# Kernel tuning notes

Hardware: AMD Instinct MI355X
Metric: run time of the kernel (lower is better)

## Reference

```python
import jax, jax.numpy as jnp
import numpy as np

D_MODEL = 1024
NUM_HEADS = 16
HEAD_DIM = D_MODEL // NUM_HEADS
B, S = 2, 2048


def setup_inputs() -> dict:
    key = jax.random.key(0)
    ks = jax.random.split(key, 6)
    scale = 0.02
    return {
        "x": jax.random.normal(ks[0], (B, S, D_MODEL), dtype=jnp.float32),
        "mask": jax.random.normal(ks[1], (S, S), dtype=jnp.float32),
        "Wqkv": jax.random.normal(ks[2], (D_MODEL, 3 * D_MODEL), dtype=jnp.float32) * scale,
        "bqkv": jax.random.normal(ks[3], (3 * D_MODEL,), dtype=jnp.float32) * scale,
        "Wout": jax.random.normal(ks[4], (D_MODEL, D_MODEL), dtype=jnp.float32) * scale,
        "bout": jax.random.normal(ks[5], (D_MODEL,), dtype=jnp.float32) * scale,
    }


def reference(x, mask, Wqkv, bqkv, Wout, bout):
    b, s, d = x.shape
    h, hd = NUM_HEADS, HEAD_DIM
    qkv = x @ Wqkv + bqkv                              # [b, s, 3d]
    qkv = qkv.reshape(b, s, h, 3 * hd).transpose(0, 2, 1, 3)  # [b, h, s, 3hd]
    q, k, v = jnp.split(qkv, 3, axis=-1)               # each [b, h, s, hd]
    scaled = jnp.einsum("bhqd,bhkd->bhqk", q, k) / jnp.sqrt(jnp.float32(hd))
    scaled = scaled + mask                             # mask [s, s] broadcasts
    attn = jax.nn.softmax(scaled, axis=-1)
    values = jnp.einsum("bhqk,bhkd->bhqd", attn, v)    # [b, h, s, hd]
    values = values.transpose(0, 2, 1, 3).reshape(b, s, d)
    return values @ Wout + bout
```

## Files before the change

kernel.cpp:

```cpp
#include <hip/hip_runtime.h>
#include <hip/hip_bf16.h>

#define D_MODEL 1024
#define NH 16
#define HD 64
#define BATCH 2
#define SEQ 2048
#define M_TOTAL (BATCH*SEQ)

typedef _Float16 f16;
typedef _Float16 half8 __attribute__((ext_vector_type(8)));
typedef _Float16 half4v __attribute__((ext_vector_type(4)));
typedef float floatx4 __attribute__((ext_vector_type(4)));

__device__ inline void gload_lds16(const void* g, void* l) {
    __builtin_amdgcn_global_load_lds(
        (const __attribute__((address_space(1))) unsigned int*)g,
        (__attribute__((address_space(3))) unsigned int*)l, 16, 0, 0);
}

__global__ void cvt_f32_f16(const float* __restrict__ src, f16* __restrict__ dst, int n4) {
    int i = blockIdx.x * blockDim.x + threadIdx.x;
    if (i < n4) {
        float4 v = ((const float4*)src)[i];
        half4v o = { (f16)v.x, (f16)v.y, (f16)v.z, (f16)v.w };
        *(half4v*)(dst + (long)i * 4) = o;
    }
}

__global__ void exp_cvt(const float* __restrict__ src, f16* __restrict__ dst, int n4) {
    int i = blockIdx.x * blockDim.x + threadIdx.x;
    if (i < n4) {
        float4 v = ((const float4*)src)[i];
        half4v o = { (f16)__expf(v.x), (f16)__expf(v.y), (f16)__expf(v.z), (f16)__expf(v.w) };
        *(half4v*)(dst + (long)i * 4) = o;
    }
}

__global__ void transpose_cvt(const float* __restrict__ src, f16* __restrict__ dst, int R, int C) {
    __shared__ float tile[32][33];
    int tx = threadIdx.x;
    int ty = threadIdx.y;
    int c0 = blockIdx.x * 32;
    int r0 = blockIdx.y * 32;
    for (int yy = 0; yy < 32; yy += 8)
        tile[ty + yy][tx] = src[(long)(r0 + ty + yy) * C + c0 + tx];
    __syncthreads();
    for (int yy = 0; yy < 32; yy += 8)
        dst[(long)(c0 + ty + yy) * R + r0 + tx] = (f16)tile[tx][ty + yy];
}

template<int MODE, int TN>
__global__ __launch_bounds__(256) void gemm_mfma(
    const f16* __restrict__ A, const f16* __restrict__ BT,
    const float* __restrict__ bias,
    f16* __restrict__ Qh, f16* __restrict__ Kh, f16* __restrict__ Vtg,
    float* __restrict__ out, int Kdim)
{
    constexpr int NF = TN / 32;
    __shared__ f16 Ah[128 * 64];
    __shared__ f16 Bh[TN * 64];
    int tid  = threadIdx.x;
    int wid  = tid >> 6;
    int lane = tid & 63;
    int quad = lane >> 4;
    int l16  = lane & 15;
    int m0 = blockIdx.y * 128;
    int n0 = blockIdx.x * TN;
    int mrow = (wid >> 1) * 64;
    int ncol = (wid & 1) * (TN / 2);
    int grow = lane >> 3;
    int gchunk = (lane & 7) ^ (grow & 7);
    int sw0 = ((quad)     ^ (l16 & 7)) * 8;
    int sw1 = ((quad + 4) ^ (l16 & 7)) * 8;

    floatx4 acc[4][NF];
    #pragma unroll
    for (int mb = 0; mb < 4; mb++)
        #pragma unroll
        for (int nb = 0; nb < NF; nb++) acc[mb][nb] = (floatx4){0.f, 0.f, 0.f, 0.f};

    const f16* Abase = A + (long)m0 * Kdim;
    const f16* Bbase = BT + (long)n0 * Kdim;

    for (int k0 = 0; k0 < Kdim; k0 += 64) {
        #pragma unroll
        for (int j = 0; j < 4; j++) {
            int r = j * 32 + wid * 8 + grow;
            gload_lds16(Abase + (long)r * Kdim + k0 + gchunk * 8, &Ah[(j * 32 + wid * 8) * 64]);
        }
        #pragma unroll
        for (int j = 0; j < TN / 32; j++) {
            int r = j * 32 + wid * 8 + grow;
            gload_lds16(Bbase + (long)r * Kdim + k0 + gchunk * 8, &Bh[(j * 32 + wid * 8) * 64]);
        }
        __syncthreads();
        #pragma unroll
        for (int h = 0; h < 2; h++) {
            int sw = h ? sw1 : sw0;
            half8 af[4];
            #pragma unroll
            for (int mb = 0; mb < 4; mb++)
                af[mb] = *(const half8*)&Ah[(mrow + mb * 16 + l16) * 64 + sw];
            #pragma unroll
            for (int nb = 0; nb < NF; nb++) {
                half8 bf = *(const half8*)&Bh[(ncol + nb * 16 + l16) * 64 + sw];
                #pragma unroll
                for (int mb = 0; mb < 4; mb++)
                    acc[mb][nb] = __builtin_amdgcn_mfma_f32_16x16x32_f16(af[mb], bf, acc[mb][nb], 0, 0, 0);
            }
        }
        __syncthreads();
    }

    #pragma unroll
    for (int nb = 0; nb < NF; nb++) {
        int n = n0 + ncol + nb * 16 + l16;
        float bv = bias[n];
        int head = 0, t = 0, d = 0;
        if (MODE == 0) { head = n / 192; int rem = n % 192; t = rem / 64; d = rem % 64; }
        #pragma unroll
        for (int mb = 0; mb < 4; mb++) {
            int mbase = m0 + mrow + mb * 16 + quad * 4;
            if (MODE == 0) {
                int b = mbase >> 11;
                int s = mbase & 2047;
                long bh = b * NH + head;
                if (t == 2) {
                    half4v pack;
                    #pragma unroll
                    for (int r = 0; r < 4; r++) pack[r] = (f16)(acc[mb][nb][r] + bv);
                    *(half4v*)&Vtg[(bh * HD + d) * SEQ + s] = pack;
                } else if (t == 0) {
                    #pragma unroll
                    for (int r = 0; r < 4; r++)
                        Qh[(bh * SEQ + s + r) * HD + d] = (f16)((acc[mb][nb][r] + bv) * 0.125f);
                } else {
                    #pragma unroll
                    for (int r = 0; r < 4; r++)
                        Kh[(bh * SEQ + s + r) * HD + d] = (f16)(acc[mb][nb][r] + bv);
                }
            } else {
                #pragma unroll
                for (int r = 0; r < 4; r++)
                    out[(long)(mbase + r) * D_MODEL + n] = acc[mb][nb][r] + bv;
            }
        }
    }
}

__global__ __launch_bounds__(256) void attn(
    const f16* __restrict__ Qh, const f16* __restrict__ Kh, const f16* __restrict__ Vtg,
    const f16* __restrict__ E, f16* __restrict__ valh)
{
    __shared__ f16 Kl[64 * 64];
    __shared__ f16 Vt[64 * 64];
    __shared__ f16 Pl[4][32 * 68];
    int tid  = threadIdx.x;
    int wid  = tid >> 6;
    int lane = tid & 63;
    int quad = lane >> 4;
    int l16  = lane & 15;
    int bh = blockIdx.y;
    int b  = bh >> 4;
    int h  = bh & 15;
    int q0 = blockIdx.x * 128 + wid * 32;

    int grow = lane >> 3;
    int gchunk = (lane & 7) ^ (grow & 7);
    int sw0 = ((quad)     ^ (l16 & 7)) * 8;
    int sw1 = ((quad + 4) ^ (l16 & 7)) * 8;

    const f16* Qbase = Qh + ((long)bh * SEQ + q0) * HD;
    half8 qf[2][2];
    #pragma unroll
    for (int m = 0; m < 2; m++)
        #pragma unroll
        for (int c = 0; c < 2; c++)
            qf[m][c] = *(const half8*)&Qbase[(long)(m * 16 + l16) * HD + c * 32 + quad * 8];

    floatx4 Of[2][4];
    float sums[2][4];
    #pragma unroll
    for (int m = 0; m < 2; m++) {
        #pragma unroll
        for (int nb = 0; nb < 4; nb++) Of[m][nb] = (floatx4){0.f, 0.f, 0.f, 0.f};
        #pragma unroll
        for (int r = 0; r < 4; r++) sums[m][r] = 0.f;
    }

    const f16* Kb = Kh + (long)bh * SEQ * HD;
    const f16* Vb = Vtg + (long)bh * HD * SEQ;

    for (int k0 = 0; k0 < SEQ; k0 += 64) {
        __syncthreads();
        #pragma unroll
        for (int j = 0; j < 2; j++) {
            int r = j * 32 + wid * 8 + grow;
            gload_lds16(Kb + (long)(k0 + r) * HD + gchunk * 8, &Kl[(j * 32 + wid * 8) * 64]);
            gload_lds16(Vb + (long)r * SEQ + k0 + gchunk * 8, &Vt[(j * 32 + wid * 8) * 64]);
        }
        __syncthreads();

        f16 ef[2][4][4];
        #pragma unroll
        for (int m = 0; m < 2; m++)
            #pragma unroll
            for (int r = 0; r < 4; r++) {
                const f16* Erow = E + (long)(q0 + m * 16 + quad * 4 + r) * SEQ + k0 + l16;
                #pragma unroll
                for (int kb = 0; kb < 4; kb++) ef[m][r][kb] = Erow[kb * 16];
            }

        floatx4 sc[2][4];
        #pragma unroll
        for (int kb = 0; kb < 4; kb++) {
            half8 kf0 = *(const half8*)&Kl[(kb * 16 + l16) * 64 + sw0];
            half8 kf1 = *(const half8*)&Kl[(kb * 16 + l16) * 64 + sw1];
            #pragma unroll
            for (int m = 0; m < 2; m++) {
                floatx4 s = (floatx4){0.f, 0.f, 0.f, 0.f};
                s = __builtin_amdgcn_mfma_f32_16x16x32_f16(qf[m][0], kf0, s, 0, 0, 0);
                s = __builtin_amdgcn_mfma_f32_16x16x32_f16(qf[m][1], kf1, s, 0, 0, 0);
                sc[m][kb] = s;
            }
        }

        #pragma unroll
        for (int m = 0; m < 2; m++)
            #pragma unroll
            for (int kb = 0; kb < 4; kb++)
                #pragma unroll
                for (int r = 0; r < 4; r++) {
                    float p = (float)ef[m][r][kb] * __expf(sc[m][kb][r]);
                    sums[m][r] += p;
                    Pl[wid][(m * 16 + quad * 4 + r) * 68 + kb * 16 + l16] = (f16)p;
                }

        half8 pf[2][2];
        #pragma unroll
        for (int m = 0; m < 2; m++)
            #pragma unroll
            for (int c = 0; c < 2; c++)
                pf[m][c] = *(const half8*)&Pl[wid][(m * 16 + l16) * 68 + c * 32 + quad * 8];

        #pragma unroll
        for (int nb = 0; nb < 4; nb++) {
            half8 vf0 = *(const half8*)&Vt[(nb * 16 + l16) * 64 + sw0];
            half8 vf1 = *(const half8*)&Vt[(nb * 16 + l16) * 64 + sw1];
            #pragma unroll
            for (int m = 0; m < 2; m++) {
                Of[m][nb] = __builtin_amdgcn_mfma_f32_16x16x32_f16(pf[m][0], vf0, Of[m][nb], 0, 0, 0);
                Of[m][nb] = __builtin_amdgcn_mfma_f32_16x16x32_f16(pf[m][1], vf1, Of[m][nb], 0, 0, 0);
            }
        }
    }

    #pragma unroll
    for (int m = 0; m < 2; m++)
        #pragma unroll
        for (int r = 0; r < 4; r++) {
            float s = sums[m][r];
            s += __shfl_xor(s, 1);
            s += __shfl_xor(s, 2);
            s += __shfl_xor(s, 4);
            s += __shfl_xor(s, 8);
            sums[m][r] = 1.f / s;
        }

    #pragma unroll
    for (int m = 0; m < 2; m++)
        #pragma unroll
        for (int nb = 0; nb < 4; nb++)
            #pragma unroll
            for (int r = 0; r < 4; r++) {
                int q = q0 + m * 16 + quad * 4 + r;
                int d = nb * 16 + l16;
                valh[((long)(b * SEQ + q)) * D_MODEL + h * HD + d] = (f16)(Of[m][nb][r] * sums[m][r]);
            }
}

extern "C" void kernel_launch(void* const* d_in, const int* in_sizes, int n_in,
                              void* d_out, int out_size, void* d_ws, size_t ws_size,
                              hipStream_t stream) {
    const float* x    = (const float*)d_in[0];
    const float* mask = (const float*)d_in[1];
    const float* Wqkv = (const float*)d_in[2];
    const float* bqkv = (const float*)d_in[3];
    const float* Wout = (const float*)d_in[4];
    const float* bout = (const float*)d_in[5];
    float* out = (float*)d_out;

    char* ws = (char*)d_ws;
    f16* xh    = (f16*)(ws + 0);
    f16* E     = (f16*)(ws + 0);
    f16* WqkvT = (f16*)(ws + 8388608);
    f16* WoutT = (f16*)(ws + 14680064);
    f16* Qh    = (f16*)(ws + 16777216);
    f16* Kh    = (f16*)(ws + 25165824);
    f16* Vtg   = (f16*)(ws + 33554432);
    f16* valh  = (f16*)(ws + 41943040);

    cvt_f32_f16<<<4096, 256, 0, stream>>>(x, xh, M_TOTAL * D_MODEL / 4);
    transpose_cvt<<<dim3(96, 32), dim3(32, 8), 0, stream>>>(Wqkv, WqkvT, 1024, 3072);
    transpose_cvt<<<dim3(32, 32), dim3(32, 8), 0, stream>>>(Wout, WoutT, 1024, 1024);
    gemm_mfma<0, 128><<<dim3(24, 32), 256, 0, stream>>>(xh, WqkvT, bqkv, Qh, Kh, Vtg, nullptr, 1024);
    exp_cvt<<<4096, 256, 0, stream>>>(mask, E, SEQ * SEQ / 4);
    attn<<<dim3(16, 32), 256, 0, stream>>>(Qh, Kh, Vtg, E, valh);
    gemm_mfma<1, 64><<<dim3(16, 32), 256, 0, stream>>>(valh, WoutT, bout, nullptr, nullptr, nullptr, out, 1024);
}
```

Baseline: 227.5 us.

## Double-buffer GEMM LDS tiles and stage mask tile via LDS in 512-thread attention

The GEMM kernel gets double-buffered LDS tiles so the next K-slice is prefetched while MFMAs run on the current one, aiming to hide global load latency behind compute. The attention kernel moves to 512 threads with 16 query rows per wave. It also loads the exp-mask tile cooperatively into LDS with async global-to-LDS copies instead of scattered per-lane 2-byte global reads. This costs more shared memory per block, which may reduce occupancy. In the GEMM, the prefetch is issued before the current buffer's reads finish, relying on the end-of-iteration barrier for correctness.

```diff
diff --git a/kernel.cpp b/kernel.cpp
--- a/kernel.cpp
+++ b/kernel.cpp
@@ -58,8 +58,8 @@
     float* __restrict__ out, int Kdim)
 {
     constexpr int NF = TN / 32;
-    __shared__ f16 Ah[128 * 64];
-    __shared__ f16 Bh[TN * 64];
+    __shared__ f16 Ah[2][128 * 64];
+    __shared__ f16 Bh[2][TN * 64];
     int tid  = threadIdx.x;
     int wid  = tid >> 6;
     int lane = tid & 63;
@@ -83,34 +83,41 @@
     const f16* Abase = A + (long)m0 * Kdim;
     const f16* Bbase = BT + (long)n0 * Kdim;
 
-    for (int k0 = 0; k0 < Kdim; k0 += 64) {
+    auto stage = [&](int buf, int k0) {
         #pragma unroll
         for (int j = 0; j < 4; j++) {
             int r = j * 32 + wid * 8 + grow;
-            gload_lds16(Abase + (long)r * Kdim + k0 + gchunk * 8, &Ah[(j * 32 + wid * 8) * 64]);
+            gload_lds16(Abase + (long)r * Kdim + k0 + gchunk * 8, &Ah[buf][(j * 32 + wid * 8) * 64]);
         }
         #pragma unroll
         for (int j = 0; j < TN / 32; j++) {
             int r = j * 32 + wid * 8 + grow;
-            gload_lds16(Bbase + (long)r * Kdim + k0 + gchunk * 8, &Bh[(j * 32 + wid * 8) * 64]);
-        }
-        __syncthreads();
+            gload_lds16(Bbase + (long)r * Kdim + k0 + gchunk * 8, &Bh[buf][(j * 32 + wid * 8) * 64]);
+        }
+    };
+
+    stage(0, 0);
+    __syncthreads();
+    int cur = 0;
+    for (int k0 = 0; k0 < Kdim; k0 += 64) {
+        if (k0 + 64 < Kdim) stage(cur ^ 1, k0 + 64);
         #pragma unroll
         for (int h = 0; h < 2; h++) {
             int sw = h ? sw1 : sw0;
             half8 af[4];
             #pragma unroll
             for (int mb = 0; mb < 4; mb++)
-                af[mb] = *(const half8*)&Ah[(mrow + mb * 16 + l16) * 64 + sw];
+                af[mb] = *(const half8*)&Ah[cur][(mrow + mb * 16 + l16) * 64 + sw];
             #pragma unroll
             for (int nb = 0; nb < NF; nb++) {
-                half8 bf = *(const half8*)&Bh[(ncol + nb * 16 + l16) * 64 + sw];
+                half8 bf = *(const half8*)&Bh[cur][(ncol + nb * 16 + l16) * 64 + sw];
                 #pragma unroll
                 for (int mb = 0; mb < 4; mb++)
                     acc[mb][nb] = __builtin_amdgcn_mfma_f32_16x16x32_f16(af[mb], bf, acc[mb][nb], 0, 0, 0);
             }
         }
         __syncthreads();
+        cur ^= 1;
     }
 
     #pragma unroll
@@ -149,13 +156,14 @@
     }
 }
 
-__global__ __launch_bounds__(256) void attn(
+__global__ __launch_bounds__(512) void attn(
     const f16* __restrict__ Qh, const f16* __restrict__ Kh, const f16* __restrict__ Vtg,
     const f16* __restrict__ E, f16* __restrict__ valh)
 {
     __shared__ f16 Kl[64 * 64];
     __shared__ f16 Vt[64 * 64];
-    __shared__ f16 Pl[4][32 * 68];
+    __shared__ f16 El[128 * 64];
+    __shared__ f16 Pl[8][16 * 68];
     int tid  = threadIdx.x;
     int wid  = tid >> 6;
     int lane = tid & 63;
@@ -164,120 +172,95 @@
     int bh = blockIdx.y;
     int b  = bh >> 4;
     int h  = bh & 15;
-    int q0 = blockIdx.x * 128 + wid * 32;
-
-    int grow = lane >> 3;
-    int gchunk = (lane & 7) ^ (grow & 7);
+    int qblk = blockIdx.x * 128;
+    int q0 = qblk + wid * 16;
+
+    int wrow = wid * 8 + (lane >> 3);
+    int kchunk = (lane & 7) ^ (wrow & 7);
     int sw0 = ((quad)     ^ (l16 & 7)) * 8;
     int sw1 = ((quad + 4) ^ (l16 & 7)) * 8;
 
     const f16* Qbase = Qh + ((long)bh * SEQ + q0) * HD;
-    half8 qf[2][2];
-    #pragma unroll
-    for (int m = 0; m < 2; m++)
-        #pragma unroll
-        for (int c = 0; c < 2; c++)
-            qf[m][c] = *(const half8*)&Qbase[(long)(m * 16 + l16) * HD + c * 32 + quad * 8];
-
-    floatx4 Of[2][4];
-    float sums[2][4];
-    #pragma unroll
-    for (int m = 0; m < 2; m++) {
-        #pragma unroll
-        for (int nb = 0; nb < 4; nb++) Of[m][nb] = (floatx4){0.f, 0.f, 0.f, 0.f};
-        #pragma unroll
-        for (int r = 0; r < 4; r++) sums[m][r] = 0.f;
-    }
+    half8 qf[2];
+    #pragma unroll
+    for (int c = 0; c < 2; c++)
+        qf[c] = *(const half8*)&Qbase[(long)l16 * HD + c * 32 + quad * 8];
+
+    floatx4 Of[4];
+    float sums[4];
+    #pragma unroll
+    for (int nb = 0; nb < 4; nb++) Of[nb] = (floatx4){0.f, 0.f, 0.f, 0.f};
+    #pragma unroll
+    for (int r = 0; r < 4; r++) sums[r] = 0.f;
 
     const f16* Kb = Kh + (long)bh * SEQ * HD;
     const f16* Vb = Vtg + (long)bh * HD * SEQ;
+    const f16* Eb = E + (long)qblk * SEQ;
 
     for (int k0 = 0; k0 < SEQ; k0 += 64) {
         __syncthreads();
-        #pragma unroll
-        for (int j = 0; j < 2; j++) {
-            int r = j * 32 + wid * 8 + grow;
-            gload_lds16(Kb + (long)(k0 + r) * HD + gchunk * 8, &Kl[(j * 32 + wid * 8) * 64]);
-            gload_lds16(Vb + (long)r * SEQ + k0 + gchunk * 8, &Vt[(j * 32 + wid * 8) * 64]);
-        }
+        gload_lds16(Kb + (long)(k0 + wrow) * HD + kchunk * 8, &Kl[(wid * 8) * 64]);
+        gload_lds16(Vb + (long)wrow * SEQ + k0 + kchunk * 8, &Vt[(wid * 8) * 64]);
+        gload_lds16(Eb + (long)wrow * SEQ + k0 + kchunk * 8, &El[(wid * 8) * 64]);
+        gload_lds16(Eb + (long)(64 + wrow) * SEQ + k0 + kchunk * 8, &El[(64 + wid * 8) * 64]);
         __syncthreads();
 
-        f16 ef[2][4][4];
-        #pragma unroll
-        for (int m = 0; m < 2; m++)
-            #pragma unroll
-            for (int r = 0; r < 4; r++) {
-                const f16* Erow = E + (long)(q0 + m * 16 + quad * 4 + r) * SEQ + k0 + l16;
-                #pragma unroll
-                for (int kb = 0; kb < 4; kb++) ef[m][r][kb] = Erow[kb * 16];
-            }
-
-        floatx4 sc[2][4];
+        floatx4 sc[4];
         #pragma unroll
         for (int kb = 0; kb < 4; kb++) {
             half8 kf0 = *(const half8*)&Kl[(kb * 16 + l16) * 64 + sw0];
             half8 kf1 = *(const half8*)&Kl[(kb * 16 + l16) * 64 + sw1];
+            floatx4 s = (floatx4){0.f, 0.f, 0.f, 0.f};
+            s = __builtin_amdgcn_mfma_f32_16x16x32_f16(qf[0], kf0, s, 0, 0, 0);
+            s = __builtin_amdgcn_mfma_f32_16x16x32_f16(qf[1], kf1, s, 0, 0, 0);
+            sc[kb] = s;
+        }
+
+        int lrow = wid * 16 + quad * 4;
+        #pragma unroll
+        for (int kb = 0; kb < 4; kb++) {
+            int cchunk = kb * 2 + (l16 >> 3);
             #pragma unroll
-            for (int m = 0; m < 2; m++) {
-                floatx4 s = (floatx4){0.f, 0.f, 0.f, 0.f};
-                s = __builtin_amdgcn_mfma_f32_16x16x32_f16(qf[m][0], kf0, s, 0, 0, 0);
-                s = __builtin_amdgcn_mfma_f32_16x16x32_f16(qf[m][1], kf1, s, 0, 0, 0);
-                sc[m][kb] = s;
+            for (int r = 0; r < 4; r++) {
+                int lr = lrow + r;
+                f16 ev = El[lr * 64 + ((cchunk ^ (lr & 7)) * 8) + (l16 & 7)];
+                float p = (float)ev * __expf(sc[kb][r]);
+                sums[r] += p;
+                Pl[wid][(quad * 4 + r) * 68 + kb * 16 + l16] = (f16)p;
             }
         }
 
-        #pragma unroll
-        for (int m = 0; m < 2; m++)
-            #pragma unroll
-            for (int kb = 0; kb < 4; kb++)
-                #pragma unroll
-                for (int r = 0; r < 4; r++) {
-                    float p = (float)ef[m][r][kb] * __expf(sc[m][kb][r]);
-                    sums[m][r] += p;
-                    Pl[wid][(m * 16 + quad * 4 + r) * 68 + kb * 16 + l16] = (f16)p;
-                }
-
-        half8 pf[2][2];
-        #pragma unroll
-        for (int m = 0; m < 2; m++)
-            #pragma unroll
-            for (int c = 0; c < 2; c++)
-                pf[m][c] = *(const half8*)&Pl[wid][(m * 16 + l16) * 68 + c * 32 + quad * 8];
+        half8 pf0 = *(const half8*)&Pl[wid][l16 * 68 + quad * 8];
+        half8 pf1 = *(const half8*)&Pl[wid][l16 * 68 + 32 + quad * 8];
 
         #pragma unroll
         for (int nb = 0; nb < 4; nb++) {
             half8 vf0 = *(const half8*)&Vt[(nb * 16 + l16) * 64 + sw0];
             half8 vf1 = *(const half8*)&Vt[(nb * 16 + l16) * 64 + sw1];
-            #pragma unroll
-            for (int m = 0; m < 2; m++) {
-                Of[m][nb] = __builtin_amdgcn_mfma_f32_16x16x32_f16(pf[m][0], vf0, Of[m][nb], 0, 0, 0);
-                Of[m][nb] = __builtin_amdgcn_mfma_f32_16x16x32_f16(pf[m][1], vf1, Of[m][nb], 0, 0, 0);
-            }
-        }
-    }
-
-    #pragma unroll
-    for (int m = 0; m < 2; m++)
+            Of[nb] = __builtin_amdgcn_mfma_f32_16x16x32_f16(pf0, vf0, Of[nb], 0, 0, 0);
+            Of[nb] = __builtin_amdgcn_mfma_f32_16x16x32_f16(pf1, vf1, Of[nb], 0, 0, 0);
+        }
+    }
+
+    float rinv[4];
+    #pragma unroll
+    for (int r = 0; r < 4; r++) {
+        float s = sums[r];
+        s += __shfl_xor(s, 1);
+        s += __shfl_xor(s, 2);
+        s += __shfl_xor(s, 4);
+        s += __shfl_xor(s, 8);
+        rinv[r] = 1.f / s;
+    }
+
+    #pragma unroll
+    for (int nb = 0; nb < 4; nb++)
         #pragma unroll
         for (int r = 0; r < 4; r++) {
-            float s = sums[m][r];
-            s += __shfl_xor(s, 1);
-            s += __shfl_xor(s, 2);
-            s += __shfl_xor(s, 4);
-            s += __shfl_xor(s, 8);
-            sums[m][r] = 1.f / s;
-        }
-
-    #pragma unroll
-    for (int m = 0; m < 2; m++)
-        #pragma unroll
-        for (int nb = 0; nb < 4; nb++)
-            #pragma unroll
-            for (int r = 0; r < 4; r++) {
-                int q = q0 + m * 16 + quad * 4 + r;
-                int d = nb * 16 + l16;
-                valh[((long)(b * SEQ + q)) * D_MODEL + h * HD + d] = (f16)(Of[m][nb][r] * sums[m][r]);
-            }
+            int q = q0 + quad * 4 + r;
+            int d = nb * 16 + l16;
+            valh[((long)(b * SEQ + q)) * D_MODEL + h * HD + d] = (f16)(Of[nb][r] * rinv[r]);
+        }
 }
 
 extern "C" void kernel_launch(void* const* d_in, const int* in_sizes, int n_in,
@@ -306,6 +289,6 @@
     transpose_cvt<<<dim3(32, 32), dim3(32, 8), 0, stream>>>(Wout, WoutT, 1024, 1024);
     gemm_mfma<0, 128><<<dim3(24, 32), 256, 0, stream>>>(xh, WqkvT, bqkv, Qh, Kh, Vtg, nullptr, 1024);
     exp_cvt<<<4096, 256, 0, stream>>>(mask, E, SEQ * SEQ / 4);
-    attn<<<dim3(16, 32), 256, 0, stream>>>(Qh, Kh, Vtg, E, valh);
+    attn<<<dim3(16, 32), 512, 0, stream>>>(Qh, Kh, Vtg, E, valh);
     gemm_mfma<1, 64><<<dim3(16, 32), 256, 0, stream>>>(valh, WoutT, bout, nullptr, nullptr, nullptr, out, 1024);
 }
```

Measured after the change: 236.1 us. +3.7%, slower.
